# Kernel tuning notes

Hardware: AMD Instinct MI355X
Metric: run time of the kernel (lower is better)

Reference implementation:

```python
import jax, jax.numpy as jnp
import numpy as np

B, L, S, H = 2, 256, 384, 768
Tc, Dc = 16, 50
WV, WD = 20000, 100
CV = 128
NEG = -1e30


def _lstm_scan(x, Wih, Whh, bih, bhh):
    # x: [N, T, D] -> hs: [N, T, Hc]; torch LSTM gate order i,f,g,o
    N = x.shape[0]
    Hc = Whh.shape[1]
    h0 = jnp.zeros((N, Hc), x.dtype)

    def step(carry, xt):
        h, c = carry
        g = xt @ Wih.T + h @ Whh.T + bih + bhh  # [N, 4Hc]
        i, f, gg, o = jnp.split(g, 4, axis=-1)
        i = jax.nn.sigmoid(i)
        f = jax.nn.sigmoid(f)
        gg = jnp.tanh(gg)
        o = jax.nn.sigmoid(o)
        c = f * c + i * gg
        h = o * jnp.tanh(c)
        return (h, c), h

    _, hs = jax.lax.scan(step, (h0, h0), jnp.swapaxes(x, 0, 1))
    return jnp.swapaxes(hs, 0, 1)


def setup_inputs() -> dict:
    key = jax.random.key(0)
    ks = jax.random.split(key, 10)
    bert_emb = jax.random.normal(ks[0], (B, S, H), jnp.float32)
    pieces2word = jax.random.randint(ks[1], (B, L, S), 0, 2, jnp.int32)
    word_ids = jax.random.randint(ks[2], (B, L), 0, WV, jnp.int32)
    char_count = jax.random.randint(ks[3], (B, L), 1, Tc + 1, jnp.int32)
    char_ids = jax.random.randint(ks[4], (B, L, Tc), 0, CV, jnp.int32)
    # mask consistent with ragged char lengths (first char_count positions valid)
    token_masks_char = (jnp.arange(Tc)[None, None, :] < char_count[..., None]).astype(jnp.int32)
    word_table = jax.random.normal(ks[5], (WV, WD), jnp.float32) * 0.02
    char_table = jax.random.normal(ks[6], (CV, Dc), jnp.float32) * 0.02
    sc = 1.0 / np.sqrt(Dc)

    def lstm_w(k):
        a, b, c, d = jax.random.split(k, 4)
        return (jax.random.uniform(a, (4 * Dc, Dc), jnp.float32, -sc, sc),
                jax.random.uniform(b, (4 * Dc, Dc), jnp.float32, -sc, sc),
                jax.random.uniform(c, (4 * Dc,), jnp.float32, -sc, sc),
                jax.random.uniform(d, (4 * Dc,), jnp.float32, -sc, sc))

    Wih_f, Whh_f, bih_f, bhh_f = lstm_w(ks[7])
    Wih_b, Whh_b, bih_b, bhh_b = lstm_w(ks[8])
    return dict(bert_emb=bert_emb, pieces2word=pieces2word, word_ids=word_ids,
                char_count=char_count, char_ids=char_ids, token_masks_char=token_masks_char,
                word_table=word_table, char_table=char_table,
                Wih_f=Wih_f, Whh_f=Whh_f, bih_f=bih_f, bhh_f=bhh_f,
                Wih_b=Wih_b, Whh_b=Whh_b, bih_b=bih_b, bhh_b=bhh_b)


def reference(bert_emb, pieces2word, word_ids, char_count, char_ids, token_masks_char,
              word_table, char_table, Wih_f, Whh_f, bih_f, bhh_f, Wih_b, Whh_b, bih_b, bhh_b):
    # --- piece2word max pool (expand + masked_fill(min) + max over pieces) ---
    minv = jnp.min(bert_emb)
    # [B, L, S, H] intermediate, as in the original expand
    masked = jnp.where(pieces2word[..., None] != 0, bert_emb[:, None, :, :], minv)
    word_reps = jnp.max(masked, axis=2)  # [B, L, H]
    # dropouts are identity in eval mode

    # --- word embedding lookup ---
    word_embed = word_table[word_ids]  # [B, L, WD]

    # --- char bi-LSTM with packed-sequence semantics ---
    lens = jnp.maximum(char_count.reshape(-1), 1)  # char_count[char_count==0]=1
    x = char_table[char_ids.reshape(B * L, Tc)]  # [N, Tc, Dc]
    h_fwd = _lstm_scan(x, Wih_f, Whh_f, bih_f, bhh_f)
    # reverse each sequence within its valid length for the backward direction
    t = jnp.arange(Tc)[None, :]
    idx = jnp.where(t < lens[:, None], lens[:, None] - 1 - t, t)  # [N, Tc]
    x_rev = jnp.take_along_axis(x, idx[..., None], axis=1)
    h_bwd = _lstm_scan(x_rev, Wih_b, Whh_b, bih_b, bhh_b)
    h_bwd = jnp.take_along_axis(h_bwd, idx[..., None], axis=1)  # back to original order
    h = jnp.concatenate([h_fwd, h_bwd], axis=-1)  # [N, Tc, 2*Dc]
    valid = (t < lens[:, None])[..., None]
    h = jnp.where(valid, h, 0.0)  # pad_packed_sequence zero-pads beyond length
    h = h.reshape(B, L, Tc, 2 * Dc)

    # --- combine(..., 'max'): masked max over ragged char groups ---
    m = jnp.where(token_masks_char[..., None] == 0, NEG, 0.0)
    sup = jnp.max(m + h, axis=2)  # [B, L, 2*Dc]
    sup = jnp.where(sup == NEG, 0.0, sup)

    return jnp.concatenate([word_reps, word_embed, sup], axis=-1)  # [B, L, H+WD+2*Dc]
```

## Files before the change

### kernel.cpp

```cpp
#include <hip/hip_runtime.h>
#include <float.h>

#define Bb 2
#define Ll 256
#define Ss 384
#define Hh 768
#define Tc 16
#define Dc 50
#define WD 100
#define CV 128
#define NG 200
#define OUTC 968


__device__ inline float tanh_fast(float x) {
    float e = __expf(2.f * x);
    return 1.f - 2.f / (e + 1.f);
}
__device__ inline float sigmoid_fast(float x) {
    return 1.f / (1.f + __expf(-x));
}


__global__ __launch_bounds__(256) void prep_kernel(
        const float* __restrict__ bert, const float* __restrict__ char_table,
        const float* __restrict__ Wih_f, const float* __restrict__ bih_f, const float* __restrict__ bhh_f,
        const float* __restrict__ Wih_b, const float* __restrict__ bih_b, const float* __restrict__ bhh_b,
        const int* __restrict__ word_ids, const float* __restrict__ word_table,
        float* __restrict__ minp, float* __restrict__ xpt, float* __restrict__ out) {
    int blk = blockIdx.x, tid = threadIdx.x;
    if (blk < 256) {
        const int n = Bb * Ss * Hh;
        float m = FLT_MAX;
        for (int i = blk * 256 + tid; i < n; i += 256 * 256) m = fminf(m, bert[i]);
        #pragma unroll
        for (int off = 32; off; off >>= 1) m = fminf(m, __shfl_down(m, off, 64));
        __shared__ float red[4];
        if ((tid & 63) == 0) red[tid >> 6] = m;
        __syncthreads();
        if (tid == 0) minp[blk] = fminf(fminf(red[0], red[1]), fminf(red[2], red[3]));
    } else if (blk < 512) {
        int idx = blk - 256;
        int dir = idx >> 7, cid = idx & 127;
        const float* Wih = dir ? Wih_b : Wih_f;
        const float* bih = dir ? bih_b : bih_f;
        const float* bhh = dir ? bhh_b : bhh_f;
        __shared__ float ct[Dc];
        if (tid < Dc) ct[tid] = char_table[cid * Dc + tid];
        __syncthreads();
        if (tid < NG) {
            float a = bih[tid] + bhh[tid];
            #pragma unroll
            for (int j = 0; j < Dc; j++) a += Wih[tid * Dc + j] * ct[j];
            xpt[idx * NG + tid] = a;
        }
    } else {
        for (int i = (blk - 512) * 256 + tid; i < Bb * Ll * WD; i += 64 * 256) {
            int bl = i / WD, d = i - bl * WD;
            out[(size_t)bl * OUTC + Hh + d] = word_table[(size_t)word_ids[bl] * WD + d];
        }
    }
}


__global__ __launch_bounds__(256) void word_kernel(
        const float* __restrict__ bert, const int* __restrict__ p2w,
        const float* __restrict__ minp, float* __restrict__ out) {
    int tid = threadIdx.x;
    __shared__ float sminv;
    if (tid < 64) {
        float m = fminf(fminf(minp[tid], minp[tid + 64]),
                        fminf(minp[tid + 128], minp[tid + 192]));
        #pragma unroll
        for (int off = 32; off; off >>= 1) m = fminf(m, __shfl_down(m, off, 64));
        if (tid == 0) sminv = m;
    }
    __syncthreads();
    int blk = blockIdx.x;
    int hc = blk % 3;
    int lt = (blk / 3) & 63;
    int b  = blk / 192;
    int h  = hc * 256 + tid;
    int l0 = lt * 4;

    float acc[4];
    #pragma unroll
    for (int i = 0; i < 4; i++) acc[i] = -FLT_MAX;

    const float* bb = bert + (size_t)b * Ss * Hh + h;
    const int*   pm = p2w + ((size_t)b * Ll + l0) * Ss;
    for (int s = 0; s < Ss; s++) {
        float v = bb[(size_t)s * Hh];
        #pragma unroll
        for (int i = 0; i < 4; i++) {
            int m = pm[i * Ss + s];
            acc[i] = fmaxf(acc[i], m ? v : -FLT_MAX);
        }
    }
    float mv = sminv;
    #pragma unroll
    for (int i = 0; i < 4; i++) {
        float a = (acc[i] == -FLT_MAX) ? mv : acc[i];
        out[((size_t)(b * Ll + l0 + i)) * OUTC + h] = a;
    }
}


__global__ __launch_bounds__(256) void lstm_kernel(
        const int* __restrict__ char_ids, const int* __restrict__ char_count,
        const float* __restrict__ Whh_f, const float* __restrict__ Whh_b,
        const float* __restrict__ xpt, float* __restrict__ out) {
    int n = blockIdx.x, dir = blockIdx.y, tid = threadIdx.x;
    const float* Whh = dir ? Whh_b : Whh_f;

    __shared__ float xg[Tc][NG];
    __shared__ float gs[NG];
    __shared__ __align__(16) float hs[52];
    __shared__ int scid[Tc];

    int len = char_count[n];
    if (len < 1) len = 1;
    if (tid < Tc) {
        int t = tid;
        int st = dir ? (t < len ? len - 1 - t : t) : t;
        scid[t] = char_ids[n * Tc + st];
    }
    if (tid < 52) hs[tid] = 0.f;
    __syncthreads();

    for (int e = tid; e < Tc * NG; e += 256) {
        int t = e / NG, g = e - t * NG;
        xg[t][g] = xpt[(dir * CV + scid[t]) * NG + g];
    }
    float w[52];
    if (tid < NG) {
        #pragma unroll
        for (int j = 0; j < Dc; j++) w[j] = Whh[tid * Dc + j];
        w[50] = 0.f; w[51] = 0.f;
    }
    __syncthreads();

    float c = 0.f, maxv = -FLT_MAX;
    for (int t = 0; t < Tc; t++) {
        if (tid < NG) {
            float g = xg[t][tid];
            #pragma unroll
            for (int j = 0; j < 52; j += 4) {
                float4 hv = *(const float4*)&hs[j];
                g += hv.x * w[j] + hv.y * w[j+1] + hv.z * w[j+2] + hv.w * w[j+3];
            }
            gs[tid] = g;
        }
        __syncthreads();
        if (tid < Dc) {
            float si = sigmoid_fast(gs[tid]);
            float sf = sigmoid_fast(gs[tid + 50]);
            float tg = tanh_fast(gs[tid + 100]);
            float so = sigmoid_fast(gs[tid + 150]);
            c = sf * c + si * tg;
            float h = so * tanh_fast(c);
            hs[tid] = h;
            if (t < len) maxv = fmaxf(maxv, h);
        }
        __syncthreads();
    }
    if (tid < Dc)
        out[(size_t)n * OUTC + (Hh + WD) + dir * Dc + tid] = maxv;
}

extern "C" void kernel_launch(void* const* d_in, const int* in_sizes, int n_in,
                              void* d_out, int out_size, void* d_ws, size_t ws_size,
                              hipStream_t stream) {
    const float* bert       = (const float*)d_in[0];
    const int*   p2w        = (const int*)d_in[1];
    const int*   word_ids   = (const int*)d_in[2];
    const int*   char_count = (const int*)d_in[3];
    const int*   char_ids   = (const int*)d_in[4];
    const float* word_table = (const float*)d_in[6];
    const float* char_table = (const float*)d_in[7];
    const float* Wih_f = (const float*)d_in[8];
    const float* Whh_f = (const float*)d_in[9];
    const float* bih_f = (const float*)d_in[10];
    const float* bhh_f = (const float*)d_in[11];
    const float* Wih_b = (const float*)d_in[12];
    const float* Whh_b = (const float*)d_in[13];
    const float* bih_b = (const float*)d_in[14];
    const float* bhh_b = (const float*)d_in[15];
    float* out = (float*)d_out;

    float* minp = (float*)d_ws;
    float* xpt  = minp + 256;

    prep_kernel<<<576, 256, 0, stream>>>(
        bert, char_table, Wih_f, bih_f, bhh_f, Wih_b, bih_b, bhh_b,
        word_ids, word_table, minp, xpt, out);
    word_kernel<<<384, 256, 0, stream>>>(bert, p2w, minp, out);
    lstm_kernel<<<dim3(512, 2), 256, 0, stream>>>(
        char_ids, char_count, Whh_f, Whh_b, xpt, out);
}
```

Baseline: 151.4 us.

## Retile word max-pool with split-S warps and batch char projection per block

The word-pooling kernel now gives each block 8 words by 128 hidden columns. Each of the four warps scans a quarter of the subword axis using float2 loads, and the partial maxima are merged through shared memory. This raises reuse of each loaded bert row across more words and branches on the mask instead of selecting. The char-table projection in the prep kernel now computes 16 characters per block with Wih held in registers, shrinking that phase from 256 blocks to 16. The costs are higher register and shared-memory use and fewer blocks in the prep kernel.

Measured after the change: 146.9 us. 1.03x faster.

```diff
diff --git a/kernel.cpp b/kernel.cpp
--- a/kernel.cpp
+++ b/kernel.cpp
@@ -39,35 +39,45 @@
         if ((tid & 63) == 0) red[tid >> 6] = m;
         __syncthreads();
         if (tid == 0) minp[blk] = fminf(fminf(red[0], red[1]), fminf(red[2], red[3]));
-    } else if (blk < 512) {
+    } else if (blk < 272) {
         int idx = blk - 256;
-        int dir = idx >> 7, cid = idx & 127;
+        int dir = idx >> 3, c0 = (idx & 7) * 16;
         const float* Wih = dir ? Wih_b : Wih_f;
         const float* bih = dir ? bih_b : bih_f;
         const float* bhh = dir ? bhh_b : bhh_f;
-        __shared__ float ct[Dc];
-        if (tid < Dc) ct[tid] = char_table[cid * Dc + tid];
+        __shared__ float ct[16][Dc];
+        for (int e = tid; e < 16 * Dc; e += 256)
+            ((float*)ct)[e] = char_table[c0 * Dc + e];
         __syncthreads();
         if (tid < NG) {
-            float a = bih[tid] + bhh[tid];
+            float w[Dc];
             #pragma unroll
-            for (int j = 0; j < Dc; j++) a += Wih[tid * Dc + j] * ct[j];
-            xpt[idx * NG + tid] = a;
+            for (int j = 0; j < Dc; j++) w[j] = Wih[tid * Dc + j];
+            float bias = bih[tid] + bhh[tid];
+            for (int cid = 0; cid < 16; cid++) {
+                float a = bias;
+                #pragma unroll
+                for (int j = 0; j < Dc; j++) a += w[j] * ct[cid][j];
+                xpt[(dir * CV + c0 + cid) * NG + tid] = a;
+            }
         }
     } else {
-        for (int i = (blk - 512) * 256 + tid; i < Bb * Ll * WD; i += 64 * 256) {
+        for (int i = (blk - 272) * 256 + tid; i < Bb * Ll * WD; i += 64 * 256) {
             int bl = i / WD, d = i - bl * WD;
             out[(size_t)bl * OUTC + Hh + d] = word_table[(size_t)word_ids[bl] * WD + d];
         }
     }
 }
 
+
+#define LT 8
 
 __global__ __launch_bounds__(256) void word_kernel(
         const float* __restrict__ bert, const int* __restrict__ p2w,
         const float* __restrict__ minp, float* __restrict__ out) {
     int tid = threadIdx.x;
     __shared__ float sminv;
+    __shared__ float sacc[4][LT][128];
     if (tid < 64) {
         float m = fminf(fminf(minp[tid], minp[tid + 64]),
                         fminf(minp[tid + 128], minp[tid + 192]));
@@ -75,33 +85,50 @@
         for (int off = 32; off; off >>= 1) m = fminf(m, __shfl_down(m, off, 64));
         if (tid == 0) sminv = m;
     }
+    int blk = blockIdx.x;
+    int hc = blk % 6;
+    int lt = (blk / 6) & 31;
+    int b  = blk / 192;
+    int l0 = lt * LT;
+    int w    = tid >> 6;
+    int lane = tid & 63;
+
+    const float2* bb2 = (const float2*)(bert + (size_t)b * Ss * Hh + hc * 128);
+    const int*    pm  = p2w + ((size_t)b * Ll + l0) * Ss;
+
+    float2 acc[LT];
+    #pragma unroll
+    for (int r = 0; r < LT; r++) { acc[r].x = -FLT_MAX; acc[r].y = -FLT_MAX; }
+
+    int s0 = w * 96;
+    for (int s = s0; s < s0 + 96; s += 4) {
+        float2 v0 = bb2[(size_t)(s + 0) * 384 + lane];
+        float2 v1 = bb2[(size_t)(s + 1) * 384 + lane];
+        float2 v2 = bb2[(size_t)(s + 2) * 384 + lane];
+        float2 v3 = bb2[(size_t)(s + 3) * 384 + lane];
+        #pragma unroll
+        for (int r = 0; r < LT; r++) {
+            const int* pr = pm + r * Ss + s;
+            if (pr[0]) { acc[r].x = fmaxf(acc[r].x, v0.x); acc[r].y = fmaxf(acc[r].y, v0.y); }
+            if (pr[1]) { acc[r].x = fmaxf(acc[r].x, v1.x); acc[r].y = fmaxf(acc[r].y, v1.y); }
+            if (pr[2]) { acc[r].x = fmaxf(acc[r].x, v2.x); acc[r].y = fmaxf(acc[r].y, v2.y); }
+            if (pr[3]) { acc[r].x = fmaxf(acc[r].x, v3.x); acc[r].y = fmaxf(acc[r].y, v3.y); }
+        }
+    }
+    #pragma unroll
+    for (int r = 0; r < LT; r++)
+        *(float2*)&sacc[w][r][lane * 2] = acc[r];
     __syncthreads();
-    int blk = blockIdx.x;
-    int hc = blk % 3;
-    int lt = (blk / 3) & 63;
-    int b  = blk / 192;
-    int h  = hc * 256 + tid;
-    int l0 = lt * 4;
-
-    float acc[4];
-    #pragma unroll
-    for (int i = 0; i < 4; i++) acc[i] = -FLT_MAX;
-
-    const float* bb = bert + (size_t)b * Ss * Hh + h;
-    const int*   pm = p2w + ((size_t)b * Ll + l0) * Ss;
-    for (int s = 0; s < Ss; s++) {
-        float v = bb[(size_t)s * Hh];
-        #pragma unroll
-        for (int i = 0; i < 4; i++) {
-            int m = pm[i * Ss + s];
-            acc[i] = fmaxf(acc[i], m ? v : -FLT_MAX);
-        }
-    }
+
     float mv = sminv;
     #pragma unroll
-    for (int i = 0; i < 4; i++) {
-        float a = (acc[i] == -FLT_MAX) ? mv : acc[i];
-        out[((size_t)(b * Ll + l0 + i)) * OUTC + h] = a;
+    for (int e = tid; e < LT * 128; e += 256) {
+        int r = e >> 7, c = e & 127;
+        float m0 = fmaxf(sacc[0][r][c], sacc[1][r][c]);
+        float m1 = fmaxf(sacc[2][r][c], sacc[3][r][c]);
+        float m  = fmaxf(m0, m1);
+        if (m == -FLT_MAX) m = mv;
+        out[((size_t)(b * Ll + l0 + r)) * OUTC + hc * 128 + c] = m;
     }
 }
 
@@ -191,7 +218,7 @@
     float* minp = (float*)d_ws;
     float* xpt  = minp + 256;
 
-    prep_kernel<<<576, 256, 0, stream>>>(
+    prep_kernel<<<336, 256, 0, stream>>>(
         bert, char_table, Wih_f, bih_f, bhh_f, Wih_b, bih_b, bhh_b,
         word_ids, word_table, minp, xpt, out);
     word_kernel<<<384, 256, 0, stream>>>(bert, p2w, minp, out);
```
